# Kernel optimization log

Hardware: AMD Instinct MI355X
Metric: run time of the kernel (lower is better)

The kernel has to match this reference:

```python
import jax, jax.numpy as jnp
import numpy as np

N = 65536
HID = 768
NH = 12
HD = HID // NH  # 64


def setup_inputs() -> dict:
    key = jax.random.key(0)
    ks = jax.random.split(key, 9)
    s = 1.0 / np.sqrt(HID)
    return {
        "x": jax.random.normal(ks[0], (N, HID), jnp.float32),
        "Wq": jax.random.normal(ks[1], (HID, HID), jnp.float32) * s,
        "bq": jax.random.normal(ks[2], (HID,), jnp.float32) * s,
        "Wk": jax.random.normal(ks[3], (HID, HID), jnp.float32) * s,
        "bk": jax.random.normal(ks[4], (HID,), jnp.float32) * s,
        "Wv": jax.random.normal(ks[5], (HID, HID), jnp.float32) * s,
        "bv": jax.random.normal(ks[6], (HID,), jnp.float32) * s,
        "Wo": jax.random.normal(ks[7], (HID, HID), jnp.float32) * s,
        "bo": jax.random.normal(ks[8], (HID,), jnp.float32) * s,
    }


def reference(x, Wq, bq, Wk, bk, Wv, bv, Wo, bo):
    # torch.nn.Linear: y = x @ W.T + b
    Q = x @ Wq.T + bq                       # [N, HID]
    K = x @ Wk.T + bk
    V = x @ Wv.T + bv
    Qh = Q.reshape(N, NH, HD)               # [N, H, D]
    Kh = K.reshape(N, HD, NH)               # [N, D, H]  (faithful to source's view)
    Vh = V.reshape(N, NH, HD)               # [N, H, D]
    # per-token head-vs-head scores: [N, H, H]
    scores = jnp.einsum('nhd,ndg->nhg', Qh, Kh) / np.sqrt(HD).astype(np.float32)
    attn = jax.nn.softmax(scores, axis=-1)  # dropout is identity in eval mode
    ctx = jnp.einsum('nhg,ngd->nhd', attn, Vh).reshape(N, HID)
    return ctx @ Wo.T + bo
```

## Files before the change

### kernel.cpp

```cpp
#include <hip/hip_runtime.h>
#include <hip/hip_bf16.h>
#include <cstdint>
#include <cstddef>

#define N_TOK 65536
#define HIDDEN 768
#define NHEAD 12
#define HEADD 64

typedef __bf16 bf16x8 __attribute__((ext_vector_type(8)));
typedef float f32x4 __attribute__((ext_vector_type(4)));

__device__ __forceinline__ float bflo(unsigned int u) {
  return __builtin_bit_cast(float, (unsigned int)(u << 16));
}
__device__ __forceinline__ float bfhi(unsigned int u) {
  return __builtin_bit_cast(float, (unsigned int)(u & 0xffff0000u));
}
__device__ __forceinline__ unsigned short f2bf(float f) {
  unsigned int x = __builtin_bit_cast(unsigned int, f);
  unsigned int r = x + 0x7fffu + ((x >> 16) & 1u);
  return (unsigned short)(r >> 16);
}

__device__ __forceinline__ void gload_lds16(const void* g, void* l) {
  __builtin_amdgcn_global_load_lds(
      (const __attribute__((address_space(1))) void*)g,
      (__attribute__((address_space(3))) void*)l, 16, 0, 0);
}

__device__ __forceinline__ bf16x8 ldsfrag(const char* base, int row, int kb) {
  int L = (row << 7) + kb;
  L ^= (row & 7) << 4;
  return *(const bf16x8*)(base + L);
}

__device__ __forceinline__ int swz(int loff) {
  return loff ^ (((loff >> 7) & 7) << 4);
}

__global__ void cvt_all_kernel(const float* __restrict__ x,
                               const float* __restrict__ Wq, const float* __restrict__ Wk,
                               const float* __restrict__ Wv, const float* __restrict__ Wo,
                               const float* __restrict__ bq, const float* __restrict__ bk,
                               const float* __restrict__ bv,
                               unsigned short* __restrict__ x_bf,
                               unsigned short* __restrict__ wqkv,
                               unsigned short* __restrict__ wo_bf,
                               float* __restrict__ bqkv) {
  const int bid = blockIdx.x;
  if (bid < 49152) {
    const int idx = bid * 256 + threadIdx.x;
    float4 v = ((const float4*)x)[idx];
    ushort4 o;
    o.x = f2bf(v.x); o.y = f2bf(v.y); o.z = f2bf(v.z); o.w = f2bf(v.w);
    ((ushort4*)x_bf)[idx] = o;
  } else if (bid < 51456) {
    const int wb = bid - 49152;
    const int mat = wb / 576;
    const int idx = (wb - mat * 576) * 256 + threadIdx.x;
    const float* src = mat == 0 ? Wq : mat == 1 ? Wk : mat == 2 ? Wv : Wo;
    unsigned short* dst = (mat == 3) ? wo_bf : wqkv + mat * (HIDDEN * HIDDEN);
    float4 v = ((const float4*)src)[idx];
    ushort4 o;
    o.x = f2bf(v.x); o.y = f2bf(v.y); o.z = f2bf(v.z); o.w = f2bf(v.w);
    ((ushort4*)dst)[idx] = o;
  } else {
    const int i = (bid - 51456) * 256 + threadIdx.x;
    if (i < 576) {
      const float* src = i < 192 ? bq : i < 384 ? bk : bv;
      const int off = i < 192 ? i : i < 384 ? i - 192 : i - 384;
      ((float4*)bqkv)[i] = ((const float4*)src)[off];
    }
  }
}

template <int MODE>
__global__ __launch_bounds__(1024)
void gemm256(const unsigned short* __restrict__ A,
             const unsigned short* __restrict__ B,
             const float* __restrict__ bias,
             void* __restrict__ C, int K, int NBLK, int ldc) {
  __shared__ __align__(16) char lds[131072];
  const int tid = threadIdx.x;
  const int lane = tid & 63;
  const int wave = tid >> 6;
  const int wr = wave >> 2;
  const int wc = wave & 3;

  const int nwg = gridDim.x;
  const int bid = blockIdx.x;
  const int wg = (bid & 7) * (nwg >> 3) + (bid >> 3);
  const int mb = wg / NBLK;
  const int nb = wg - mb * NBLK;
  const int brow = mb << 8;
  const int bcol = nb << 8;

  const int Ld = tid * 16;
  const int Ls = Ld ^ (((tid >> 3) & 7) << 4);
  const int sr = Ls >> 7;
  const int sc = (Ls & 127) >> 1;

  const int NT = K >> 6;

#define STAGE(Mat, panelRow, bufbase, matoff, half, kt)                         \
  do {                                                                          \
    const unsigned short* _s =                                                  \
        (Mat) + (size_t)((panelRow) + (half) * 128 + sr) * K + ((kt) << 6) + sc;\
    char* _d = (char*)lds + (bufbase) + (matoff) + ((half) << 14) + Ld;         \
    gload_lds16(_s, _d);                                                        \
  } while (0)

  f32x4 acc[4][4];
#pragma unroll
  for (int m = 0; m < 4; ++m)
#pragma unroll
    for (int n = 0; n < 4; ++n) acc[m][n] = (f32x4){0.f, 0.f, 0.f, 0.f};

  const int arow = wr * 64 + (lane & 15);
  const int nrow = wc * 64 + (lane & 15);
  const int kpart = (lane >> 4) * 16;

  STAGE(A, brow, 0, 0, 0, 0);
  STAGE(A, brow, 0, 0, 1, 0);
  STAGE(B, bcol, 0, 32768, 0, 0);
  STAGE(B, bcol, 0, 32768, 1, 0);
  if (NT > 1) {
    STAGE(A, brow, 65536, 0, 0, 1);
    STAGE(A, brow, 65536, 0, 1, 1);
    asm volatile("s_waitcnt vmcnt(2)" ::: "memory");
  } else {
    asm volatile("s_waitcnt vmcnt(0)" ::: "memory");
  }
  __builtin_amdgcn_s_barrier();

  for (int t = 0; t < NT; ++t) {
    const int cur = t & 1;
    const char* la = lds + cur * 65536;
    const char* lb = la + 32768;
    const int sbuf = cur * 65536;
    const int obuf = (cur ^ 1) * 65536;

    bf16x8 aF[4], bLo[2], bHi[2];

#pragma unroll
    for (int m = 0; m < 4; ++m) aF[m] = ldsfrag(la, arow + m * 16, kpart);
#pragma unroll
    for (int n = 0; n < 2; ++n) bLo[n] = ldsfrag(lb, nrow + n * 16, kpart);
    if (t + 1 < NT) {
      STAGE(B, bcol, obuf, 32768, 0, t + 1);
      STAGE(B, bcol, obuf, 32768, 1, t + 1);
    }
    __builtin_amdgcn_s_barrier();
    asm volatile("s_waitcnt lgkmcnt(0)" ::: "memory");
    __builtin_amdgcn_sched_barrier(0);
    __builtin_amdgcn_s_setprio(1);
#pragma unroll
    for (int m = 0; m < 4; ++m)
#pragma unroll
      for (int n = 0; n < 2; ++n)
        acc[m][n] = __builtin_amdgcn_mfma_f32_16x16x32_bf16(aF[m], bLo[n],
                                                            acc[m][n], 0, 0, 0);
    __builtin_amdgcn_s_setprio(0);

#pragma unroll
    for (int n = 0; n < 2; ++n) bHi[n] = ldsfrag(lb, nrow + 32 + n * 16, kpart);
    __builtin_amdgcn_s_barrier();
    asm volatile("s_waitcnt lgkmcnt(0)" ::: "memory");
    __builtin_amdgcn_sched_barrier(0);
    __builtin_amdgcn_s_setprio(1);
#pragma unroll
    for (int m = 0; m < 4; ++m)
#pragma unroll
      for (int n = 0; n < 2; ++n)
        acc[m][n + 2] = __builtin_amdgcn_mfma_f32_16x16x32_bf16(
            aF[m], bHi[n], acc[m][n + 2], 0, 0, 0);
    __builtin_amdgcn_s_setprio(0);

#pragma unroll
    for (int m = 0; m < 4; ++m) aF[m] = ldsfrag(la, arow + m * 16, 64 + kpart);
#pragma unroll
    for (int n = 0; n < 2; ++n) bLo[n] = ldsfrag(lb, nrow + n * 16, 64 + kpart);
    __builtin_amdgcn_s_barrier();
    asm volatile("s_waitcnt lgkmcnt(0)" ::: "memory");
    __builtin_amdgcn_sched_barrier(0);
    __builtin_amdgcn_s_setprio(1);
#pragma unroll
    for (int m = 0; m < 4; ++m)
#pragma unroll
      for (int n = 0; n < 2; ++n)
        acc[m][n] = __builtin_amdgcn_mfma_f32_16x16x32_bf16(aF[m], bLo[n],
                                                            acc[m][n], 0, 0, 0);
    __builtin_amdgcn_s_setprio(0);

#pragma unroll
    for (int n = 0; n < 2; ++n)
      bHi[n] = ldsfrag(lb, nrow + 32 + n * 16, 64 + kpart);
    if (t + 2 < NT) {
      STAGE(A, brow, sbuf, 0, 0, t + 2);
      STAGE(A, brow, sbuf, 0, 1, t + 2);
      asm volatile("s_waitcnt vmcnt(2)" ::: "memory");
    } else {
      asm volatile("s_waitcnt vmcnt(0)" ::: "memory");
    }
    __builtin_amdgcn_s_barrier();
    asm volatile("s_waitcnt lgkmcnt(0)" ::: "memory");
    __builtin_amdgcn_sched_barrier(0);
    __builtin_amdgcn_s_setprio(1);
#pragma unroll
    for (int m = 0; m < 4; ++m)
#pragma unroll
      for (int n = 0; n < 2; ++n)
        acc[m][n + 2] = __builtin_amdgcn_mfma_f32_16x16x32_bf16(
            aF[m], bHi[n], acc[m][n + 2], 0, 0, 0);
    __builtin_amdgcn_s_setprio(0);
  }
#undef STAGE

  const int crow0 = brow + wr * 64 + (lane >> 4) * 4;
  const int ccol0 = bcol + wc * 64 + (lane & 15);
#pragma unroll
  for (int m = 0; m < 4; ++m) {
#pragma unroll
    for (int n = 0; n < 4; ++n) {
      const int col = ccol0 + n * 16;
      const float bv = bias[col];
#pragma unroll
      for (int r = 0; r < 4; ++r) {
        const int row = crow0 + m * 16 + r;
        const float v = acc[m][n][r] + bv;
        if (MODE == 1)
          ((float*)C)[(size_t)row * ldc + col] = v;
        else
          ((unsigned short*)C)[(size_t)row * ldc + col] = f2bf(v);
      }
    }
  }
}

#define T_BLK 8
#define ROWB 4624

__global__ __launch_bounds__(128)
void attn_kernel(const unsigned short* __restrict__ qkv,
                 unsigned short* __restrict__ ctx) {
  __shared__ __align__(16) char lds[T_BLK * ROWB];
  const int tid = threadIdx.x;
  const int blk = blockIdx.x;

  const uint4* src = (const uint4*)(qkv + (size_t)blk * (T_BLK * 2304));
#pragma unroll
  for (int it = 0; it < 18; ++it) {
    const int l = it * 128 + tid;
    const uint4 v = src[l];
    const int tok = l / 288;
    const int loff = (l - tok * 288) * 16;
    *(uint4*)(lds + tok * ROWB + swz(loff)) = v;
  }
  __syncthreads();

  const int tok = tid / 12;
  const int h = tid - tok * 12;
  const bool active = (tid < 96);
  const char* rowb = lds + tok * ROWB;

  float p[12];
  if (active) {
    float s[12];
#pragma unroll
    for (int g = 0; g < 12; ++g) s[g] = 0.f;
#pragma unroll
    for (int c = 0; c < 8; ++c) {
      const uint4 qc = *(const uint4*)(rowb + swz(h * 128 + c * 16));
      const unsigned int qw[4] = {qc.x, qc.y, qc.z, qc.w};
      float qd[8];
#pragma unroll
      for (int w = 0; w < 4; ++w) {
        qd[2 * w] = bflo(qw[w]);
        qd[2 * w + 1] = bfhi(qw[w]);
      }
#pragma unroll
      for (int j = 0; j < 8; ++j) {
        const int koff = 1536 + (c * 8 + j) * 24;
        const uint2 k0 = *(const uint2*)(rowb + swz(koff));
        const uint2 k1 = *(const uint2*)(rowb + swz(koff + 8));
        const uint2 k2 = *(const uint2*)(rowb + swz(koff + 16));
        const float q = qd[j];
        s[0] += q * bflo(k0.x);  s[1] += q * bfhi(k0.x);
        s[2] += q * bflo(k0.y);  s[3] += q * bfhi(k0.y);
        s[4] += q * bflo(k1.x);  s[5] += q * bfhi(k1.x);
        s[6] += q * bflo(k1.y);  s[7] += q * bfhi(k1.y);
        s[8] += q * bflo(k2.x);  s[9] += q * bfhi(k2.x);
        s[10] += q * bflo(k2.y); s[11] += q * bfhi(k2.y);
      }
    }
    float mx = s[0];
#pragma unroll
    for (int g = 1; g < 12; ++g) mx = fmaxf(mx, s[g]);
    float sum = 0.f;
#pragma unroll
    for (int g = 0; g < 12; ++g) {
      p[g] = __expf((s[g] - mx) * 0.125f);
      sum += p[g];
    }
    const float inv = 1.0f / sum;
#pragma unroll
    for (int g = 0; g < 12; ++g) p[g] *= inv;
  }

  __syncthreads();

  if (active) {
    char* qpark = lds + tok * ROWB;
#pragma unroll
    for (int c = 0; c < 8; ++c) {
      float o[8];
#pragma unroll
      for (int k = 0; k < 8; ++k) o[k] = 0.f;
#pragma unroll
      for (int g = 0; g < 12; ++g) {
        const uint4 vv = *(const uint4*)(rowb + swz(3072 + g * 128 + c * 16));
        const unsigned int vw[4] = {vv.x, vv.y, vv.z, vv.w};
#pragma unroll
        for (int k = 0; k < 4; ++k) {
          o[2 * k] += p[g] * bflo(vw[k]);
          o[2 * k + 1] += p[g] * bfhi(vw[k]);
        }
      }
      uint4 w;
      w.x = (unsigned int)f2bf(o[0]) | ((unsigned int)f2bf(o[1]) << 16);
      w.y = (unsigned int)f2bf(o[2]) | ((unsigned int)f2bf(o[3]) << 16);
      w.z = (unsigned int)f2bf(o[4]) | ((unsigned int)f2bf(o[5]) << 16);
      w.w = (unsigned int)f2bf(o[6]) | ((unsigned int)f2bf(o[7]) << 16);
      *(uint4*)(qpark + swz(h * 128 + c * 16)) = w;
    }
  }
  __syncthreads();

  uint4* dst = (uint4*)(ctx + (size_t)blk * (T_BLK * 768));
#pragma unroll
  for (int it = 0; it < 6; ++it) {
    const int l = it * 128 + tid;
    const int tok2 = l / 96;
    const int boff = (l - tok2 * 96) * 16;
    dst[l] = *(const uint4*)(lds + tok2 * ROWB + swz(boff));
  }
}

extern "C" void kernel_launch(void* const* d_in, const int* in_sizes, int n_in,
                              void* d_out, int out_size, void* d_ws, size_t ws_size,
                              hipStream_t stream) {
  const float* x = (const float*)d_in[0];
  const float* Wq = (const float*)d_in[1];
  const float* bq = (const float*)d_in[2];
  const float* Wk = (const float*)d_in[3];
  const float* bk = (const float*)d_in[4];
  const float* Wv = (const float*)d_in[5];
  const float* bv = (const float*)d_in[6];
  const float* Wo = (const float*)d_in[7];
  const float* bo = (const float*)d_in[8];
  float* out = (float*)d_out;

  char* ws = (char*)d_ws;
  unsigned short* x_bf = (unsigned short*)ws;
  unsigned short* ctx = (unsigned short*)ws;
  unsigned short* qkv = (unsigned short*)(ws + 100663296u);
  unsigned short* wqkv = (unsigned short*)(ws + 402653184u);
  unsigned short* wo_bf = (unsigned short*)(ws + 406192128u);
  float* bqkv = (float*)(ws + 407371776u);

  cvt_all_kernel<<<51459, 256, 0, stream>>>(x, Wq, Wk, Wv, Wo, bq, bk, bv,
                                            x_bf, wqkv, wo_bf, bqkv);

  gemm256<0><<<(N_TOK / 256) * (2304 / 256), 1024, 0, stream>>>(
      x_bf, wqkv, bqkv, qkv, HIDDEN, 2304 / 256, 2304);

  attn_kernel<<<N_TOK / T_BLK, 128, 0, stream>>>(qkv, ctx);

  gemm256<1><<<(N_TOK / 256) * (HIDDEN / 256), 1024, 0, stream>>>(
      ctx, wo_bf, bo, out, HIDDEN, HIDDEN / 256, HIDDEN);
}
```

Baseline: 506.0 us.

## Fuse fp32-to-bf16 activation conversion into QKV GEMM A-tile loading

Drops the separate pass that converted x to bf16. A new GEMM mode loads fp32 x directly into registers, packs it to bf16 and writes it to LDS, while the weight tiles still use direct global-to-LDS loads. This removes a full read and write of the activation tensor, plus a big launch. In exchange, each column-block workgroup now reads fp32 rather than bf16 A tiles, which doubles A-side load traffic. The A prefetch also drops from two stages ahead to one and waits on vmcnt(0), which may expose latency.

```diff
diff --git a/kernel.cpp b/kernel.cpp
--- a/kernel.cpp
+++ b/kernel.cpp
@@ -22,6 +22,9 @@
   unsigned int r = x + 0x7fffu + ((x >> 16) & 1u);
   return (unsigned short)(r >> 16);
 }
+__device__ __forceinline__ unsigned int pk2bf(float a, float b) {
+  return (unsigned int)f2bf(a) | ((unsigned int)f2bf(b) << 16);
+}
 
 __device__ __forceinline__ void gload_lds16(const void* g, void* l) {
   __builtin_amdgcn_global_load_lds(
@@ -39,26 +42,17 @@
   return loff ^ (((loff >> 7) & 7) << 4);
 }
 
-__global__ void cvt_all_kernel(const float* __restrict__ x,
-                               const float* __restrict__ Wq, const float* __restrict__ Wk,
-                               const float* __restrict__ Wv, const float* __restrict__ Wo,
-                               const float* __restrict__ bq, const float* __restrict__ bk,
-                               const float* __restrict__ bv,
-                               unsigned short* __restrict__ x_bf,
-                               unsigned short* __restrict__ wqkv,
-                               unsigned short* __restrict__ wo_bf,
-                               float* __restrict__ bqkv) {
+__global__ void cvtw_kernel(const float* __restrict__ Wq, const float* __restrict__ Wk,
+                            const float* __restrict__ Wv, const float* __restrict__ Wo,
+                            const float* __restrict__ bq, const float* __restrict__ bk,
+                            const float* __restrict__ bv,
+                            unsigned short* __restrict__ wqkv,
+                            unsigned short* __restrict__ wo_bf,
+                            float* __restrict__ bqkv) {
   const int bid = blockIdx.x;
-  if (bid < 49152) {
-    const int idx = bid * 256 + threadIdx.x;
-    float4 v = ((const float4*)x)[idx];
-    ushort4 o;
-    o.x = f2bf(v.x); o.y = f2bf(v.y); o.z = f2bf(v.z); o.w = f2bf(v.w);
-    ((ushort4*)x_bf)[idx] = o;
-  } else if (bid < 51456) {
-    const int wb = bid - 49152;
-    const int mat = wb / 576;
-    const int idx = (wb - mat * 576) * 256 + threadIdx.x;
+  if (bid < 2304) {
+    const int mat = bid / 576;
+    const int idx = (bid - mat * 576) * 256 + threadIdx.x;
     const float* src = mat == 0 ? Wq : mat == 1 ? Wk : mat == 2 ? Wv : Wo;
     unsigned short* dst = (mat == 3) ? wo_bf : wqkv + mat * (HIDDEN * HIDDEN);
     float4 v = ((const float4*)src)[idx];
@@ -66,7 +60,7 @@
     o.x = f2bf(v.x); o.y = f2bf(v.y); o.z = f2bf(v.z); o.w = f2bf(v.w);
     ((ushort4*)dst)[idx] = o;
   } else {
-    const int i = (bid - 51456) * 256 + threadIdx.x;
+    const int i = (bid - 2304) * 256 + threadIdx.x;
     if (i < 576) {
       const float* src = i < 192 ? bq : i < 384 ? bk : bv;
       const int off = i < 192 ? i : i < 384 ? i - 192 : i - 384;
@@ -77,10 +71,11 @@
 
 template <int MODE>
 __global__ __launch_bounds__(1024)
-void gemm256(const unsigned short* __restrict__ A,
-             const unsigned short* __restrict__ B,
+void gemm256(const void* __restrict__ Av, const unsigned short* __restrict__ B,
              const float* __restrict__ bias,
              void* __restrict__ C, int K, int NBLK, int ldc) {
+  const unsigned short* A = (const unsigned short*)Av;
+  const float* Af = (const float*)Av;
   __shared__ __align__(16) char lds[131072];
   const int tid = threadIdx.x;
   const int lane = tid & 63;
@@ -121,16 +116,33 @@
   const int nrow = wc * 64 + (lane & 15);
   const int kpart = (lane >> 4) * 16;
 
-  STAGE(A, brow, 0, 0, 0, 0);
-  STAGE(A, brow, 0, 0, 1, 0);
-  STAGE(B, bcol, 0, 32768, 0, 0);
-  STAGE(B, bcol, 0, 32768, 1, 0);
-  if (NT > 1) {
-    STAGE(A, brow, 65536, 0, 0, 1);
-    STAGE(A, brow, 65536, 0, 1, 1);
-    asm volatile("s_waitcnt vmcnt(2)" ::: "memory");
+  if (MODE == 2) {
+    const float* s0 = Af + (size_t)(brow + sr) * K + sc;
+    const float* s1 = s0 + (size_t)128 * K;
+    float4 p0 = ((const float4*)s0)[0], p1 = ((const float4*)s0)[1];
+    float4 p2 = ((const float4*)s1)[0], p3 = ((const float4*)s1)[1];
+    STAGE(B, bcol, 0, 32768, 0, 0);
+    STAGE(B, bcol, 0, 32768, 1, 0);
+    uint4 w0, w1;
+    w0.x = pk2bf(p0.x, p0.y); w0.y = pk2bf(p0.z, p0.w);
+    w0.z = pk2bf(p1.x, p1.y); w0.w = pk2bf(p1.z, p1.w);
+    w1.x = pk2bf(p2.x, p2.y); w1.y = pk2bf(p2.z, p2.w);
+    w1.z = pk2bf(p3.x, p3.y); w1.w = pk2bf(p3.z, p3.w);
+    *(uint4*)(lds + Ld) = w0;
+    *(uint4*)(lds + 16384 + Ld) = w1;
+    asm volatile("s_waitcnt vmcnt(0) lgkmcnt(0)" ::: "memory");
   } else {
-    asm volatile("s_waitcnt vmcnt(0)" ::: "memory");
+    STAGE(A, brow, 0, 0, 0, 0);
+    STAGE(A, brow, 0, 0, 1, 0);
+    STAGE(B, bcol, 0, 32768, 0, 0);
+    STAGE(B, bcol, 0, 32768, 1, 0);
+    if (NT > 1) {
+      STAGE(A, brow, 65536, 0, 0, 1);
+      STAGE(A, brow, 65536, 0, 1, 1);
+      asm volatile("s_waitcnt vmcnt(2)" ::: "memory");
+    } else {
+      asm volatile("s_waitcnt vmcnt(0)" ::: "memory");
+    }
   }
   __builtin_amdgcn_s_barrier();
 
@@ -142,6 +154,7 @@
     const int obuf = (cur ^ 1) * 65536;
 
     bf16x8 aF[4], bLo[2], bHi[2];
+    float4 a4[4];
 
 #pragma unroll
     for (int m = 0; m < 4; ++m) aF[m] = ldsfrag(la, arow + m * 16, kpart);
@@ -150,6 +163,14 @@
     if (t + 1 < NT) {
       STAGE(B, bcol, obuf, 32768, 0, t + 1);
       STAGE(B, bcol, obuf, 32768, 1, t + 1);
+      if (MODE == 2) {
+        const float* s0 = Af + (size_t)(brow + sr) * K + (t + 1) * 64 + sc;
+        const float* s1 = s0 + (size_t)128 * K;
+        a4[0] = ((const float4*)s0)[0];
+        a4[1] = ((const float4*)s0)[1];
+        a4[2] = ((const float4*)s1)[0];
+        a4[3] = ((const float4*)s1)[1];
+      }
     }
     __builtin_amdgcn_s_barrier();
     asm volatile("s_waitcnt lgkmcnt(0)" ::: "memory");
@@ -196,16 +217,32 @@
 #pragma unroll
     for (int n = 0; n < 2; ++n)
       bHi[n] = ldsfrag(lb, nrow + 32 + n * 16, 64 + kpart);
-    if (t + 2 < NT) {
-      STAGE(A, brow, sbuf, 0, 0, t + 2);
-      STAGE(A, brow, sbuf, 0, 1, t + 2);
-      asm volatile("s_waitcnt vmcnt(2)" ::: "memory");
+    if (MODE == 2) {
+      if (t + 1 < NT) {
+        asm volatile("s_waitcnt vmcnt(0)" ::: "memory");
+        uint4 w0, w1;
+        w0.x = pk2bf(a4[0].x, a4[0].y); w0.y = pk2bf(a4[0].z, a4[0].w);
+        w0.z = pk2bf(a4[1].x, a4[1].y); w0.w = pk2bf(a4[1].z, a4[1].w);
+        w1.x = pk2bf(a4[2].x, a4[2].y); w1.y = pk2bf(a4[2].z, a4[2].w);
+        w1.z = pk2bf(a4[3].x, a4[3].y); w1.w = pk2bf(a4[3].z, a4[3].w);
+        *(uint4*)(lds + obuf + Ld) = w0;
+        *(uint4*)(lds + obuf + 16384 + Ld) = w1;
+      }
+      asm volatile("s_waitcnt lgkmcnt(0)" ::: "memory");
+      __builtin_amdgcn_s_barrier();
+      __builtin_amdgcn_sched_barrier(0);
     } else {
-      asm volatile("s_waitcnt vmcnt(0)" ::: "memory");
-    }
-    __builtin_amdgcn_s_barrier();
-    asm volatile("s_waitcnt lgkmcnt(0)" ::: "memory");
-    __builtin_amdgcn_sched_barrier(0);
+      if (t + 2 < NT) {
+        STAGE(A, brow, sbuf, 0, 0, t + 2);
+        STAGE(A, brow, sbuf, 0, 1, t + 2);
+        asm volatile("s_waitcnt vmcnt(2)" ::: "memory");
+      } else {
+        asm volatile("s_waitcnt vmcnt(0)" ::: "memory");
+      }
+      __builtin_amdgcn_s_barrier();
+      asm volatile("s_waitcnt lgkmcnt(0)" ::: "memory");
+      __builtin_amdgcn_sched_barrier(0);
+    }
     __builtin_amdgcn_s_setprio(1);
 #pragma unroll
     for (int m = 0; m < 4; ++m)
@@ -362,18 +399,17 @@
   float* out = (float*)d_out;
 
   char* ws = (char*)d_ws;
-  unsigned short* x_bf = (unsigned short*)ws;
   unsigned short* ctx = (unsigned short*)ws;
   unsigned short* qkv = (unsigned short*)(ws + 100663296u);
   unsigned short* wqkv = (unsigned short*)(ws + 402653184u);
   unsigned short* wo_bf = (unsigned short*)(ws + 406192128u);
   float* bqkv = (float*)(ws + 407371776u);
 
-  cvt_all_kernel<<<51459, 256, 0, stream>>>(x, Wq, Wk, Wv, Wo, bq, bk, bv,
-                                            x_bf, wqkv, wo_bf, bqkv);
-
-  gemm256<0><<<(N_TOK / 256) * (2304 / 256), 1024, 0, stream>>>(
-      x_bf, wqkv, bqkv, qkv, HIDDEN, 2304 / 256, 2304);
+  cvtw_kernel<<<2307, 256, 0, stream>>>(Wq, Wk, Wv, Wo, bq, bk, bv,
+                                        wqkv, wo_bf, bqkv);
+
+  gemm256<2><<<(N_TOK / 256) * (2304 / 256), 1024, 0, stream>>>(
+      x, wqkv, bqkv, qkv, HIDDEN, 2304 / 256, 2304);
 
   attn_kernel<<<N_TOK / T_BLK, 128, 0, stream>>>(qkv, ctx);
 
```

Result: slower. 2.017 ms (+298.5%).
